# Kernel optimization log

Hardware: AMD Instinct MI355X
Metric: run time of the kernel (lower is better)

The kernel has to match this reference:

```python
import jax, jax.numpy as jnp
import numpy as np

N = 50000
E = 800000
D_IN = 128
D_H = 128
D_OUT = 40
BN_EPS = 1e-5


def setup_inputs() -> dict:
    key = jax.random.key(0)
    ks = jax.random.split(key, 16)
    s = lambda d: 1.0 / np.sqrt(d)
    inp = {
        "x": jax.random.normal(ks[0], (N, D_IN), jnp.float32),
        "edge_index": jax.random.randint(ks[1], (2, E), 0, N, jnp.int64),
        # conv1 MLP: Linear(D_IN,D_H) -> BN -> ReLU -> Linear(D_H,D_H) -> ReLU
        "W1a": jax.random.uniform(ks[2], (D_IN, D_H), jnp.float32, -s(D_IN), s(D_IN)),
        "b1a": jnp.zeros((D_H,), jnp.float32),
        "g1": jnp.ones((D_H,), jnp.float32),
        "be1": jnp.zeros((D_H,), jnp.float32),
        "W2a": jax.random.uniform(ks[3], (D_H, D_H), jnp.float32, -s(D_H), s(D_H)),
        "b2a": jnp.zeros((D_H,), jnp.float32),
        # conv2 MLP
        "W1b": jax.random.uniform(ks[4], (D_H, D_H), jnp.float32, -s(D_H), s(D_H)),
        "b1b": jnp.zeros((D_H,), jnp.float32),
        "g2": jnp.ones((D_H,), jnp.float32),
        "be2": jnp.zeros((D_H,), jnp.float32),
        "W2b": jax.random.uniform(ks[5], (D_H, D_H), jnp.float32, -s(D_H), s(D_H)),
        "b2b": jnp.zeros((D_H,), jnp.float32),
        # head
        "Wl1": jax.random.uniform(ks[6], (D_H, D_H), jnp.float32, -s(D_H), s(D_H)),
        "bl1": jnp.zeros((D_H,), jnp.float32),
        "Wl2": jax.random.uniform(ks[7], (D_H, D_OUT), jnp.float32, -s(D_H), s(D_H)),
        "bl2": jnp.zeros((D_OUT,), jnp.float32),
    }
    return inp


def _batchnorm(h, gamma, beta):
    # BatchNorm1d in training mode: biased batch stats over the node dim
    mu = h.mean(axis=0)
    var = h.var(axis=0)
    return (h - mu) * jax.lax.rsqrt(var + BN_EPS) * gamma + beta


def _gin_conv(x, src, dst, W1, b1, gamma, beta, W2, b2):
    # sum-aggregation over neighbors (eps = 0): (1+eps)*x + sum_{j in N(i)} x_j
    agg = x + jax.ops.segment_sum(x[src], dst, num_segments=N)
    h = agg @ W1 + b1
    h = jax.nn.relu(_batchnorm(h, gamma, beta))
    return jax.nn.relu(h @ W2 + b2)


def reference(x, edge_index, W1a, b1a, g1, be1, W2a, b2a,
              W1b, b1b, g2, be2, W2b, b2b, Wl1, bl1, Wl2, bl2):
    src, dst = edge_index[0], edge_index[1]
    h = jax.nn.relu(_gin_conv(x, src, dst, W1a, b1a, g1, be1, W2a, b2a))
    # dropout is a no-op here (deterministic reference / eval)
    h = _gin_conv(h, src, dst, W1b, b1b, g2, be2, W2b, b2b)
    h = jax.nn.relu(h @ Wl1 + bl1)
    h = h @ Wl2 + bl2
    return jax.nn.log_softmax(h, axis=1)
```

## Files before the change

### kernel.cpp

```cpp
#include <hip/hip_runtime.h>
#include <math.h>

#define NN 50000
#define NE 800000
#define DD 128
#define DOUT 40
#define BN_EPS_F 1e-5f
#define BSTRIDE 32
#define OVF_MAX 8192
#define NPX (NN / 8)
#define EPB 1024
#define BUCKET_BLOCKS (((NE + EPB - 1) / EPB) * 8)
#define X2BF_BLOCKS 6250
#define WPREP_BLOCKS ((5 * 16384 + 255) / 256)
#define NSLOT 8

typedef __attribute__((ext_vector_type(8))) short bf16x8;
typedef __attribute__((ext_vector_type(4))) float f32x4;

static __device__ __forceinline__ unsigned short f2bf(float f) {
  unsigned u = __float_as_uint(f);
  unsigned r = (u + 0x7FFFu + ((u >> 16) & 1u)) >> 16;
  return (unsigned short)r;
}
static __device__ __forceinline__ float bf2f(unsigned short u) {
  return __uint_as_float((unsigned)u << 16);
}

__global__ void k_zero(int* __restrict__ cnt, float* __restrict__ stats,
                       int* __restrict__ ovfc) {
  int i = blockIdx.x * 256 + threadIdx.x;
  if (i < NN) cnt[i] = 0;
  if (i < 2 * NSLOT * 2 * DD) stats[i] = 0.f;
  if (i == 0) ovfc[0] = 0;
}

__global__ void k_bucketprep(const int* __restrict__ srcI, const int* __restrict__ dstI,
                             int* __restrict__ cnt, unsigned short* __restrict__ bkt,
                             int* __restrict__ ovfc, unsigned* __restrict__ ovf,
                             const float4* __restrict__ x, ushort4* __restrict__ xb,
                             const float* __restrict__ W0, const float* __restrict__ W1,
                             const float* __restrict__ W2, const float* __restrict__ W3,
                             const float* __restrict__ W4, unsigned short* __restrict__ wf) {
  int b = blockIdx.x;
  if (b < BUCKET_BLOCKS) {
    int xcd = b & 7;
    int chunk = b >> 3;
    int lo = xcd * NPX, hi = lo + NPX;
    int e0 = chunk * EPB + threadIdx.x * 4;
    if (e0 < NE) {
      int4 d4 = *(const int4*)(dstI + e0);
      int4 s4 = *(const int4*)(srcI + e0);
      int dd[4] = {d4.x, d4.y, d4.z, d4.w};
      int ss[4] = {s4.x, s4.y, s4.z, s4.w};
#pragma unroll
      for (int i = 0; i < 4; i++) {
        int d = dd[i];
        if (d >= lo && d < hi) {
          int r = atomicAdd(&cnt[d], 1);
          if (r < BSTRIDE) {
            bkt[(size_t)d * BSTRIDE + r] = (unsigned short)ss[i];
          } else {
            int o = atomicAdd(ovfc, 1);
            if (o < OVF_MAX) ovf[o] = ((unsigned)d << 16) | (unsigned)ss[i];
          }
        }
      }
    }
  } else if (b < BUCKET_BLOCKS + X2BF_BLOCKS) {
    int i = (b - BUCKET_BLOCKS) * 256 + threadIdx.x;
    if (i < NN * 32) {
      float4 v = x[i];
      ushort4 r;
      r.x = f2bf(v.x); r.y = f2bf(v.y); r.z = f2bf(v.z); r.w = f2bf(v.w);
      xb[i] = r;
    }
  } else {
    int fid = (b - BUCKET_BLOCKS - X2BF_BLOCKS) * 256 + threadIdx.x;
    if (fid >= 5 * 16384) return;
    int g = fid >> 14;
    int r = fid & 16383;
    int i = r & 7;
    int lane = (r >> 3) & 63;
    int ks = (r >> 9) & 3;
    int ct = r >> 11;
    int k = ks * 32 + (lane >> 4) * 8 + i;
    int col = ct * 16 + (lane & 15);
    const float* Wp = (g == 0) ? W0 : (g == 1) ? W1 : (g == 2) ? W2 : (g == 3) ? W3 : W4;
    float w = Wp[k * DD + col];
    wf[g * 16384 + r] = f2bf(w);
  }
}

__global__ void k_aggr_bf(const ushort4* __restrict__ x, const int* __restrict__ cnt,
                          const unsigned short* __restrict__ bkt,
                          const int* __restrict__ ovfc, const unsigned* __restrict__ ovf,
                          ushort4* __restrict__ out) {
  int tid = blockIdx.x * 256 + threadIdx.x;
  int node = tid >> 5;
  if (node >= NN) return;
  int c = tid & 31;
  int cn = cnt[node];
  int ce = (cn < BSTRIDE) ? cn : BSTRIDE;
  const unsigned short* bp = bkt + (size_t)node * BSTRIDE;
  ushort4 sv = x[node * 32 + c];
  float ax = bf2f(sv.x), ay = bf2f(sv.y), az = bf2f(sv.z), aw = bf2f(sv.w);
  int j = 0;
  for (; j + 3 < ce; j += 4) {
    int s0 = bp[j], s1 = bp[j + 1], s2 = bp[j + 2], s3 = bp[j + 3];
    ushort4 v0 = x[s0 * 32 + c];
    ushort4 v1 = x[s1 * 32 + c];
    ushort4 v2 = x[s2 * 32 + c];
    ushort4 v3 = x[s3 * 32 + c];
    ax += bf2f(v0.x) + bf2f(v1.x) + bf2f(v2.x) + bf2f(v3.x);
    ay += bf2f(v0.y) + bf2f(v1.y) + bf2f(v2.y) + bf2f(v3.y);
    az += bf2f(v0.z) + bf2f(v1.z) + bf2f(v2.z) + bf2f(v3.z);
    aw += bf2f(v0.w) + bf2f(v1.w) + bf2f(v2.w) + bf2f(v3.w);
  }
  for (; j < ce; j++) {
    int s0 = bp[j];
    ushort4 v0 = x[s0 * 32 + c];
    ax += bf2f(v0.x); ay += bf2f(v0.y); az += bf2f(v0.z); aw += bf2f(v0.w);
  }
  if (cn > BSTRIDE) {
    int no = ovfc[0];
    if (no > OVF_MAX) no = OVF_MAX;
    for (int o = 0; o < no; o++) {
      unsigned pr = ovf[o];
      if ((int)(pr >> 16) == node) {
        ushort4 v0 = x[(int)(pr & 0xFFFFu) * 32 + c];
        ax += bf2f(v0.x); ay += bf2f(v0.y); az += bf2f(v0.z); aw += bf2f(v0.w);
      }
    }
  }
  ushort4 r;
  r.x = f2bf(ax); r.y = f2bf(ay); r.z = f2bf(az); r.w = f2bf(aw);
  out[node * 32 + c] = r;
}

template<bool BN_IN, bool RELU_OUT, bool STATS_OUT, bool HEAD>
__global__ __launch_bounds__(512) void k_mgemm(
    const unsigned short* __restrict__ in, const unsigned short* __restrict__ wf,
    const float* __restrict__ bias, float* __restrict__ outF,
    unsigned short* __restrict__ outB,
    const float* __restrict__ statsIn, float* __restrict__ statsOut,
    const float* __restrict__ gamma, const float* __restrict__ beta,
    const float* __restrict__ W2h, const float* __restrict__ b2h) {
  constexpr int SMEM_BYTES = HEAD ? 54272 : 32768;
  __shared__ __align__(16) char smem[SMEM_BYTES];
  __shared__ float scs[DD], shs[DD], lbias[DD], ls[DD], lq[DD];
  short* lw = (short*)smem;
  int tid = threadIdx.x;
  int lane = tid & 63, wv = tid >> 6;
  int rbase = blockIdx.x * 128 + wv * 16;
  int kq = (lane >> 4) * 8;

  bf16x8 araw[4];
  {
    int row = rbase + (lane & 15);
    bool v = row < NN;
    const unsigned short* ap = in + (size_t)row * DD + kq;
    bf16x8 zz = {0, 0, 0, 0, 0, 0, 0, 0};
#pragma unroll
    for (int ks = 0; ks < 4; ks++)
      araw[ks] = v ? *(const bf16x8*)(ap + ks * 32) : zz;
  }

  {
    const float4* src = (const float4*)wf;
    float4* dst = (float4*)lw;
#pragma unroll
    for (int it = 0; it < 4; it++) dst[it * 512 + tid] = src[it * 512 + tid];
  }
  if (tid < DD) {
    lbias[tid] = bias[tid];
    if (STATS_OUT) { ls[tid] = 0.f; lq[tid] = 0.f; }
    if (BN_IN) {
      float su = 0.f, sq = 0.f;
#pragma unroll
      for (int s = 0; s < NSLOT; s++) {
        su += statsIn[s * 2 * DD + tid];
        sq += statsIn[s * 2 * DD + DD + tid];
      }
      float mu  = su * (1.0f / NN);
      float var = sq * (1.0f / NN) - mu * mu;
      float sc  = gamma[tid] * rsqrtf(var + BN_EPS_F);
      scs[tid] = sc;
      shs[tid] = beta[tid] - mu * sc;
    }
  }
  __syncthreads();

  bf16x8 ahi[4];
  if constexpr (BN_IN) {
#pragma unroll
    for (int ks = 0; ks < 4; ks++) {
      const float4* s4 = (const float4*)&scs[ks * 32 + kq];
      const float4* h4 = (const float4*)&shs[ks * 32 + kq];
      float4 sa = s4[0], sb = s4[1], ha = h4[0], hb = h4[1];
      float ss[8] = {sa.x, sa.y, sa.z, sa.w, sb.x, sb.y, sb.z, sb.w};
      float hh[8] = {ha.x, ha.y, ha.z, ha.w, hb.x, hb.y, hb.z, hb.w};
      bf16x8 h;
#pragma unroll
      for (int i = 0; i < 8; i++) {
        float xv = fmaxf(bf2f((unsigned short)araw[ks][i]) * ss[i] + hh[i], 0.f);
        h[i] = (short)f2bf(xv);
      }
      ahi[ks] = h;
    }
  } else {
#pragma unroll
    for (int ks = 0; ks < 4; ks++) ahi[ks] = araw[ks];
  }

  f32x4 acc[8];
#pragma unroll
  for (int ct = 0; ct < 8; ct++) acc[ct] = (f32x4){0.f, 0.f, 0.f, 0.f};
  const bf16x8* lwv = (const bf16x8*)lw;
#pragma unroll
  for (int ks = 0; ks < 4; ks++) {
#pragma unroll
    for (int ct = 0; ct < 8; ct++) {
      bf16x8 bh = lwv[(ct * 4 + ks) * 64 + lane];
      acc[ct] = __builtin_amdgcn_mfma_f32_16x16x32_bf16(ahi[ks], bh, acc[ct], 0, 0, 0);
    }
  }

  if constexpr (!HEAD) {
    int r0 = rbase + (lane >> 4) * 4;
#pragma unroll
    for (int ct = 0; ct < 8; ct++) {
      int col = ct * 16 + (lane & 15);
      float bb = lbias[col];
      float s = 0.f, q = 0.f;
#pragma unroll
      for (int j = 0; j < 4; j++) {
        int row = r0 + j;
        if (row < NN) {
          float v = acc[ct][j] + bb;
          if (RELU_OUT) v = fmaxf(v, 0.f);
          outB[(size_t)row * DD + col] = f2bf(v);
          if (STATS_OUT) { s += v; q += v * v; }
        }
      }
      if (STATS_OUT) {
        s += __shfl_xor(s, 16); s += __shfl_xor(s, 32);
        q += __shfl_xor(q, 16); q += __shfl_xor(q, 32);
        if ((lane >> 4) == 0) {
          atomicAdd(&ls[col], s);
          atomicAdd(&lq[col], q);
        }
      }
    }
    if (STATS_OUT) {
      __syncthreads();
      if (tid < DD) {
        float* slot = statsOut + (blockIdx.x & (NSLOT - 1)) * 2 * DD;
        atomicAdd(&slot[tid], ls[tid]);
        atomicAdd(&slot[DD + tid], lq[tid]);
      }
    }
  } else {
    unsigned short* hs = (unsigned short*)smem;
    float* W2s = (float*)(smem + 33792);
    __syncthreads();
    {
      int lr0 = wv * 16 + (lane >> 4) * 4;
#pragma unroll
      for (int ct = 0; ct < 8; ct++) {
        int col = ct * 16 + (lane & 15);
        float bb = lbias[col];
#pragma unroll
        for (int j = 0; j < 4; j++) {
          float v = fmaxf(acc[ct][j] + bb, 0.f);
          hs[(lr0 + j) * 132 + col] = f2bf(v);
        }
      }
      const float4* W2g = (const float4*)W2h;
      float4* W2s4 = (float4*)W2s;
#pragma unroll
      for (int it = 0; it < 3; it++) {
        int idx = it * 512 + tid;
        if (idx < 1280) W2s4[idx] = W2g[idx];
      }
    }
    __syncthreads();
    int lrow = tid >> 2, q = tid & 3;
    int grow = blockIdx.x * 128 + lrow;
    float a2[40];
#pragma unroll
    for (int j = 0; j < 40; j++) a2[j] = 0.f;
    for (int kk = 0; kk < 32; kk++) {
      int k = kk * 4 + q;
      float hv = bf2f(hs[lrow * 132 + k]);
      const float4* wrow = (const float4*)(W2s + k * DOUT);
#pragma unroll
      for (int j4 = 0; j4 < 10; j4++) {
        float4 w = wrow[j4];
        a2[j4 * 4 + 0] += hv * w.x;
        a2[j4 * 4 + 1] += hv * w.y;
        a2[j4 * 4 + 2] += hv * w.z;
        a2[j4 * 4 + 3] += hv * w.w;
      }
    }
#pragma unroll
    for (int j = 0; j < 40; j++) {
      a2[j] += __shfl_xor(a2[j], 1);
      a2[j] += __shfl_xor(a2[j], 2);
    }
    if (q == 0 && grow < NN) {
      const float4* b24 = (const float4*)b2h;
      float m = -INFINITY;
#pragma unroll
      for (int j4 = 0; j4 < 10; j4++) {
        float4 bb = b24[j4];
        a2[j4 * 4 + 0] += bb.x; a2[j4 * 4 + 1] += bb.y;
        a2[j4 * 4 + 2] += bb.z; a2[j4 * 4 + 3] += bb.w;
      }
#pragma unroll
      for (int j = 0; j < 40; j++) m = fmaxf(m, a2[j]);
      float s = 0.f;
#pragma unroll
      for (int j = 0; j < 40; j++) s += expf(a2[j] - m);
      float d = m + logf(s);
      float4* out4 = (float4*)(outF + (size_t)grow * DOUT);
#pragma unroll
      for (int j4 = 0; j4 < 10; j4++) {
        float4 v = make_float4(a2[j4 * 4 + 0] - d, a2[j4 * 4 + 1] - d,
                               a2[j4 * 4 + 2] - d, a2[j4 * 4 + 3] - d);
        out4[j4] = v;
      }
    }
  }
}

extern "C" void kernel_launch(void* const* d_in, const int* in_sizes, int n_in,
                              void* d_out, int out_size, void* d_ws, size_t ws_size,
                              hipStream_t stream) {
  const float* x   = (const float*)d_in[0];
  const int*   ei  = (const int*)d_in[1];
  const float* W1a = (const float*)d_in[2];
  const float* b1a = (const float*)d_in[3];
  const float* g1  = (const float*)d_in[4];
  const float* be1 = (const float*)d_in[5];
  const float* W2a = (const float*)d_in[6];
  const float* b2a = (const float*)d_in[7];
  const float* W1b = (const float*)d_in[8];
  const float* b1b = (const float*)d_in[9];
  const float* g2  = (const float*)d_in[10];
  const float* be2 = (const float*)d_in[11];
  const float* W2b = (const float*)d_in[12];
  const float* b2b = (const float*)d_in[13];
  const float* Wl1 = (const float*)d_in[14];
  const float* bl1 = (const float*)d_in[15];
  const float* Wl2 = (const float*)d_in[16];
  const float* bl2 = (const float*)d_in[17];
  float* out = (float*)d_out;

  unsigned short* bufX = (unsigned short*)d_ws;
  unsigned short* bufA = bufX + (size_t)NN * DD;
  unsigned short* bufB = bufA + (size_t)NN * DD;
  float* stats1 = (float*)(bufB + (size_t)NN * DD);
  float* stats2 = stats1 + NSLOT * 2 * DD;
  int*   cnt    = (int*)(stats2 + NSLOT * 2 * DD);
  int*   ovfc   = cnt + NN;
  unsigned* ovf = (unsigned*)(ovfc + 4);
  unsigned short* bkt = (unsigned short*)(ovf + OVF_MAX);
  size_t wfOff = (((size_t)(bkt + (size_t)NN * BSTRIDE) - (size_t)d_ws) + 15) & ~(size_t)15;
  unsigned short* wfrag = (unsigned short*)((char*)d_ws + wfOff);

  const int* srcI = ei;
  const int* dstI = ei + NE;

  dim3 blk(256);
  int aggrGrid = (NN * 32 + 255) / 256;
  int gemmGrid = (NN + 127) / 128;
  int bpGrid   = BUCKET_BLOCKS + X2BF_BLOCKS + WPREP_BLOCKS;
  int zeroGrid = (NN + 255) / 256;

  k_zero<<<zeroGrid, blk, 0, stream>>>(cnt, stats1, ovfc);
  k_bucketprep<<<bpGrid, blk, 0, stream>>>(srcI, dstI, cnt, bkt, ovfc, ovf,
                                           (const float4*)x, (ushort4*)bufX,
                                           W1a, W2a, W1b, W2b, Wl1, wfrag);

  k_aggr_bf<<<aggrGrid, blk, 0, stream>>>((const ushort4*)bufX, cnt, bkt, ovfc, ovf,
                                          (ushort4*)bufA);
  k_mgemm<false, false, true, false><<<gemmGrid, 512, 0, stream>>>(
      bufA, wfrag + 0 * 16384, b1a, nullptr, bufB,
      nullptr, stats1, nullptr, nullptr, nullptr, nullptr);
  k_mgemm<true, true, false, false><<<gemmGrid, 512, 0, stream>>>(
      bufB, wfrag + 1 * 16384, b2a, nullptr, bufA,
      stats1, nullptr, g1, be1, nullptr, nullptr);
  k_aggr_bf<<<aggrGrid, blk, 0, stream>>>((const ushort4*)bufA, cnt, bkt, ovfc, ovf,
                                          (ushort4*)bufB);
  k_mgemm<false, false, true, false><<<gemmGrid, 512, 0, stream>>>(
      bufB, wfrag + 2 * 16384, b1b, nullptr, bufA,
      nullptr, stats2, nullptr, nullptr, nullptr, nullptr);
  k_mgemm<true, true, false, false><<<gemmGrid, 512, 0, stream>>>(
      bufA, wfrag + 3 * 16384, b2b, nullptr, bufB,
      stats2, nullptr, g2, be2, nullptr, nullptr);
  k_mgemm<false, false, true, true><<<gemmGrid, 512, 0, stream>>>(
      bufB, wfrag + 4 * 16384, bl1, out, nullptr,
      nullptr, nullptr, nullptr, nullptr, Wl2, bl2);
}
```

Measured before the change: 191.8 us.

## Fuse neighbor aggregation with first GIN linear layer and BN stats

Replaces the separate aggregation kernel and the first MLP GEMM with one kernel that gathers neighbor rows into shared memory (16-byte bf16x8 loads per lane) and immediately runs the MFMA GEMM, bias and BN-statistic accumulation on them. This removes the write and re-read of the aggregated activation buffer and one launch per conv layer. It also turns off stats accumulation in the head GEMM, which was unused. The cost is smaller 64-row blocks that each reload the full 32 KB weight tile, and a larger shared-memory footprint that may lower occupancy during the latency-bound gather phase.

Result: no change. 192.4 us (+0.3%).

```diff
diff --git a/kernel.cpp b/kernel.cpp
--- a/kernel.cpp
+++ b/kernel.cpp
@@ -14,6 +14,7 @@
 #define X2BF_BLOCKS 6250
 #define WPREP_BLOCKS ((5 * 16384 + 255) / 256)
 #define NSLOT 8
+#define HST 136
 
 typedef __attribute__((ext_vector_type(8))) short bf16x8;
 typedef __attribute__((ext_vector_type(4))) float f32x4;
@@ -92,50 +93,132 @@
   }
 }
 
-__global__ void k_aggr_bf(const ushort4* __restrict__ x, const int* __restrict__ cnt,
-                          const unsigned short* __restrict__ bkt,
-                          const int* __restrict__ ovfc, const unsigned* __restrict__ ovf,
-                          ushort4* __restrict__ out) {
-  int tid = blockIdx.x * 256 + threadIdx.x;
-  int node = tid >> 5;
-  if (node >= NN) return;
-  int c = tid & 31;
-  int cn = cnt[node];
-  int ce = (cn < BSTRIDE) ? cn : BSTRIDE;
-  const unsigned short* bp = bkt + (size_t)node * BSTRIDE;
-  ushort4 sv = x[node * 32 + c];
-  float ax = bf2f(sv.x), ay = bf2f(sv.y), az = bf2f(sv.z), aw = bf2f(sv.w);
-  int j = 0;
-  for (; j + 3 < ce; j += 4) {
-    int s0 = bp[j], s1 = bp[j + 1], s2 = bp[j + 2], s3 = bp[j + 3];
-    ushort4 v0 = x[s0 * 32 + c];
-    ushort4 v1 = x[s1 * 32 + c];
-    ushort4 v2 = x[s2 * 32 + c];
-    ushort4 v3 = x[s3 * 32 + c];
-    ax += bf2f(v0.x) + bf2f(v1.x) + bf2f(v2.x) + bf2f(v3.x);
-    ay += bf2f(v0.y) + bf2f(v1.y) + bf2f(v2.y) + bf2f(v3.y);
-    az += bf2f(v0.z) + bf2f(v1.z) + bf2f(v2.z) + bf2f(v3.z);
-    aw += bf2f(v0.w) + bf2f(v1.w) + bf2f(v2.w) + bf2f(v3.w);
-  }
-  for (; j < ce; j++) {
-    int s0 = bp[j];
-    ushort4 v0 = x[s0 * 32 + c];
-    ax += bf2f(v0.x); ay += bf2f(v0.y); az += bf2f(v0.z); aw += bf2f(v0.w);
-  }
-  if (cn > BSTRIDE) {
-    int no = ovfc[0];
-    if (no > OVF_MAX) no = OVF_MAX;
-    for (int o = 0; o < no; o++) {
-      unsigned pr = ovf[o];
-      if ((int)(pr >> 16) == node) {
-        ushort4 v0 = x[(int)(pr & 0xFFFFu) * 32 + c];
-        ax += bf2f(v0.x); ay += bf2f(v0.y); az += bf2f(v0.z); aw += bf2f(v0.w);
-      }
-    }
-  }
-  ushort4 r;
-  r.x = f2bf(ax); r.y = f2bf(ay); r.z = f2bf(az); r.w = f2bf(aw);
-  out[node * 32 + c] = r;
+__global__ __launch_bounds__(512) void k_aggemm(
+    const unsigned short* __restrict__ in, const int* __restrict__ cnt,
+    const unsigned short* __restrict__ bkt,
+    const int* __restrict__ ovfc, const unsigned* __restrict__ ovf,
+    const unsigned short* __restrict__ wf, const float* __restrict__ bias,
+    unsigned short* __restrict__ outB, float* __restrict__ statsOut) {
+  __shared__ __align__(16) short lw[16384];
+  __shared__ __align__(16) unsigned short hs[64 * HST];
+  __shared__ float lbias[DD], ls[DD], lq[DD];
+  int tid = threadIdx.x;
+  int lane = tid & 63, wv = tid >> 6;
+  int rbase = blockIdx.x * 64;
+
+  {
+    const float4* src = (const float4*)wf;
+    float4* dst = (float4*)lw;
+#pragma unroll
+    for (int it = 0; it < 4; it++) dst[it * 512 + tid] = src[it * 512 + tid];
+  }
+  if (tid < DD) { lbias[tid] = bias[tid]; ls[tid] = 0.f; lq[tid] = 0.f; }
+
+  {
+    int l16 = tid & 15;
+    const unsigned short* base = in + l16 * 8;
+#pragma unroll
+    for (int rep = 0; rep < 2; rep++) {
+      int nl = (tid >> 4) + rep * 32;
+      int node = rbase + nl;
+      float a[8] = {0.f, 0.f, 0.f, 0.f, 0.f, 0.f, 0.f, 0.f};
+      if (node < NN) {
+        bf16x8 sv = *(const bf16x8*)(base + (size_t)node * DD);
+#pragma unroll
+        for (int i = 0; i < 8; i++) a[i] = bf2f((unsigned short)sv[i]);
+        int cn = cnt[node];
+        int ce = (cn < BSTRIDE) ? cn : BSTRIDE;
+        const unsigned short* bp = bkt + (size_t)node * BSTRIDE;
+        int j = 0;
+        for (; j + 3 < ce; j += 4) {
+          int s0 = bp[j], s1 = bp[j + 1], s2 = bp[j + 2], s3 = bp[j + 3];
+          bf16x8 v0 = *(const bf16x8*)(base + (size_t)s0 * DD);
+          bf16x8 v1 = *(const bf16x8*)(base + (size_t)s1 * DD);
+          bf16x8 v2 = *(const bf16x8*)(base + (size_t)s2 * DD);
+          bf16x8 v3 = *(const bf16x8*)(base + (size_t)s3 * DD);
+#pragma unroll
+          for (int i = 0; i < 8; i++)
+            a[i] += bf2f((unsigned short)v0[i]) + bf2f((unsigned short)v1[i]) +
+                    bf2f((unsigned short)v2[i]) + bf2f((unsigned short)v3[i]);
+        }
+        for (; j < ce; j++) {
+          bf16x8 v0 = *(const bf16x8*)(base + (size_t)bp[j] * DD);
+#pragma unroll
+          for (int i = 0; i < 8; i++) a[i] += bf2f((unsigned short)v0[i]);
+        }
+        if (cn > BSTRIDE) {
+          int no = ovfc[0];
+          if (no > OVF_MAX) no = OVF_MAX;
+          for (int o = 0; o < no; o++) {
+            unsigned pr = ovf[o];
+            if ((int)(pr >> 16) == node) {
+              bf16x8 v0 = *(const bf16x8*)(base + (size_t)(pr & 0xFFFFu) * DD);
+#pragma unroll
+              for (int i = 0; i < 8; i++) a[i] += bf2f((unsigned short)v0[i]);
+            }
+          }
+        }
+      }
+      bf16x8 hv;
+#pragma unroll
+      for (int i = 0; i < 8; i++) hv[i] = (short)f2bf(a[i]);
+      *(bf16x8*)(&hs[nl * HST + l16 * 8]) = hv;
+    }
+  }
+  __syncthreads();
+
+  int rblk = wv >> 1, ch = wv & 1;
+  int kq = (lane >> 4) * 8;
+  bf16x8 araw[4];
+  {
+    int lr = rblk * 16 + (lane & 15);
+#pragma unroll
+    for (int ks = 0; ks < 4; ks++)
+      araw[ks] = *(const bf16x8*)(&hs[lr * HST + ks * 32 + kq]);
+  }
+  f32x4 acc[4];
+#pragma unroll
+  for (int ct = 0; ct < 4; ct++) acc[ct] = (f32x4){0.f, 0.f, 0.f, 0.f};
+  const bf16x8* lwv = (const bf16x8*)lw;
+#pragma unroll
+  for (int ks = 0; ks < 4; ks++) {
+#pragma unroll
+    for (int ct = 0; ct < 4; ct++) {
+      bf16x8 bh = lwv[((ch * 4 + ct) * 4 + ks) * 64 + lane];
+      acc[ct] = __builtin_amdgcn_mfma_f32_16x16x32_bf16(araw[ks], bh, acc[ct], 0, 0, 0);
+    }
+  }
+
+  {
+    int r0 = rbase + rblk * 16 + (lane >> 4) * 4;
+#pragma unroll
+    for (int ct = 0; ct < 4; ct++) {
+      int col = ch * 64 + ct * 16 + (lane & 15);
+      float bb = lbias[col];
+      float s = 0.f, q = 0.f;
+#pragma unroll
+      for (int j = 0; j < 4; j++) {
+        int row = r0 + j;
+        if (row < NN) {
+          float v = acc[ct][j] + bb;
+          outB[(size_t)row * DD + col] = f2bf(v);
+          s += v; q += v * v;
+        }
+      }
+      s += __shfl_xor(s, 16); s += __shfl_xor(s, 32);
+      q += __shfl_xor(q, 16); q += __shfl_xor(q, 32);
+      if ((lane >> 4) == 0) {
+        atomicAdd(&ls[col], s);
+        atomicAdd(&lq[col], q);
+      }
+    }
+  }
+  __syncthreads();
+  if (tid < DD) {
+    float* slot = statsOut + (blockIdx.x & (NSLOT - 1)) * 2 * DD;
+    atomicAdd(&slot[tid], ls[tid]);
+    atomicAdd(&slot[DD + tid], lq[tid]);
+  }
 }
 
 template<bool BN_IN, bool RELU_OUT, bool STATS_OUT, bool HEAD>
@@ -261,7 +344,7 @@
       }
     }
   } else {
-    unsigned short* hs = (unsigned short*)smem;
+    unsigned short* hs2 = (unsigned short*)smem;
     float* W2s = (float*)(smem + 33792);
     __syncthreads();
     {
@@ -273,7 +356,7 @@
 #pragma unroll
         for (int j = 0; j < 4; j++) {
           float v = fmaxf(acc[ct][j] + bb, 0.f);
-          hs[(lr0 + j) * 132 + col] = f2bf(v);
+          hs2[(lr0 + j) * 132 + col] = f2bf(v);
         }
       }
       const float4* W2g = (const float4*)W2h;
@@ -292,7 +375,7 @@
     for (int j = 0; j < 40; j++) a2[j] = 0.f;
     for (int kk = 0; kk < 32; kk++) {
       int k = kk * 4 + q;
-      float hv = bf2f(hs[lrow * 132 + k]);
+      float hv = bf2f(hs2[lrow * 132 + k]);
       const float4* wrow = (const float4*)(W2s + k * DOUT);
 #pragma unroll
       for (int j4 = 0; j4 < 10; j4++) {
@@ -373,8 +456,8 @@
   const int* dstI = ei + NE;
 
   dim3 blk(256);
-  int aggrGrid = (NN * 32 + 255) / 256;
   int gemmGrid = (NN + 127) / 128;
+  int agGrid   = (NN + 63) / 64;
   int bpGrid   = BUCKET_BLOCKS + X2BF_BLOCKS + WPREP_BLOCKS;
   int zeroGrid = (NN + 255) / 256;
 
@@ -383,23 +466,17 @@
                                            (const float4*)x, (ushort4*)bufX,
                                            W1a, W2a, W1b, W2b, Wl1, wfrag);
 
-  k_aggr_bf<<<aggrGrid, blk, 0, stream>>>((const ushort4*)bufX, cnt, bkt, ovfc, ovf,
-                                          (ushort4*)bufA);
-  k_mgemm<false, false, true, false><<<gemmGrid, 512, 0, stream>>>(
-      bufA, wfrag + 0 * 16384, b1a, nullptr, bufB,
-      nullptr, stats1, nullptr, nullptr, nullptr, nullptr);
+  k_aggemm<<<agGrid, 512, 0, stream>>>(bufX, cnt, bkt, ovfc, ovf,
+                                       wfrag + 0 * 16384, b1a, bufB, stats1);
   k_mgemm<true, true, false, false><<<gemmGrid, 512, 0, stream>>>(
       bufB, wfrag + 1 * 16384, b2a, nullptr, bufA,
       stats1, nullptr, g1, be1, nullptr, nullptr);
-  k_aggr_bf<<<aggrGrid, blk, 0, stream>>>((const ushort4*)bufA, cnt, bkt, ovfc, ovf,
-                                          (ushort4*)bufB);
-  k_mgemm<false, false, true, false><<<gemmGrid, 512, 0, stream>>>(
-      bufB, wfrag + 2 * 16384, b1b, nullptr, bufA,
-      nullptr, stats2, nullptr, nullptr, nullptr, nullptr);
+  k_aggemm<<<agGrid, 512, 0, stream>>>(bufA, cnt, bkt, ovfc, ovf,
+                                       wfrag + 2 * 16384, b1b, bufB, stats2);
   k_mgemm<true, true, false, false><<<gemmGrid, 512, 0, stream>>>(
-      bufA, wfrag + 3 * 16384, b2b, nullptr, bufB,
+      bufB, wfrag + 3 * 16384, b2b, nullptr, bufA,
       stats2, nullptr, g2, be2, nullptr, nullptr);
-  k_mgemm<false, false, true, true><<<gemmGrid, 512, 0, stream>>>(
-      bufB, wfrag + 4 * 16384, bl1, out, nullptr,
+  k_mgemm<false, false, false, true><<<gemmGrid, 512, 0, stream>>>(
+      bufA, wfrag + 4 * 16384, bl1, out, nullptr,
       nullptr, nullptr, nullptr, nullptr, Wl2, bl2);
 }
```
